# Kernel tuning notes

Hardware: AMD Instinct MI355X
Metric: run time of the kernel (lower is better)

The kernel has to match this reference:

```python
import jax, jax.numpy as jnp
import numpy as np

N_NODES = 100000
N_EDGES = 1000000  # even: first half = 'in' direction, second half = 'out' (inverse) direction
H = 128
N_REL = 200        # num_relations (for rel_labels embedding)
N_RELG = 100       # num_rel_graph; edge_type in [0, 2*N_RELG)
N_GRAPHS = 256
N_CLS = 2


def _glorot(key, shape):
    s = (6.0 / (shape[0] + shape[1])) ** 0.5
    return jax.random.uniform(key, shape, jnp.float32, -s, s)


def setup_inputs() -> dict:
    key = jax.random.key(0)
    ks = jax.random.split(key, 32)
    inp = {}
    inp['x'] = jax.random.normal(ks[0], (N_NODES, H), jnp.float32)
    inp['edge_index'] = jax.random.randint(ks[1], (2, N_EDGES), 0, N_NODES)
    inp['edge_type'] = jax.random.randint(ks[2], (N_EDGES,), 0, 2 * N_RELG)
    inp['batch'] = jnp.sort(jax.random.randint(ks[3], (N_NODES,), 0, N_GRAPHS))
    inp['rel_labels'] = jax.random.randint(ks[4], (N_GRAPHS,), 0, N_REL)
    inp['drop_prob'] = 0  # eval mode -> dropout is identity
    # learned parameters
    inp['rel_emb_table'] = jax.random.normal(ks[5], (N_REL, H), jnp.float32)
    inp['rel_graph_emb'] = _glorot(ks[6], (N_RELG, H))
    i = 7
    for l in (1, 2, 3):
        for nm in ('w_in', 'w_out', 'w_loop', 'w_rel'):
            inp[f'{nm}{l}'] = _glorot(ks[i], (H, H)); i += 1
        inp[f'loop_rel{l}'] = _glorot(ks[i], (1, H)); i += 1
        inp[f'b{l}'] = jnp.zeros((H,), jnp.float32)
    inp['lin_w'] = _glorot(ks[i], (2 * H, N_CLS))
    inp['lin_b'] = jnp.zeros((N_CLS,), jnp.float32)
    return inp


def _conv(x, edge_index, edge_type, rel, w_in, w_out, w_loop, w_rel, loop_rel, b):
    """CompGCNConv with 'sub' composition, tanh activation (BN/dropout identity in eval)."""
    n = x.shape[0]
    rel_all = jnp.concatenate([rel, loop_rel], axis=0)  # append loop relation
    half = edge_index.shape[1] // 2

    def direction(idx, etyp, w):
        src, dst = idx[0], idx[1]
        # norm as in CompGCN: deg over row(src), norm = deg_inv[row]*deg_inv[col]
        deg = jax.ops.segment_sum(jnp.ones(src.shape[0], x.dtype), src, num_segments=n)
        dinv = jnp.where(deg > 0, deg ** -0.5, 0.0)
        norm = dinv[src] * dinv[dst]                      # [E/2]
        msg = ((x[src] - rel_all[etyp]) @ w) * norm[:, None]  # gather-compose-transform
        return jax.ops.segment_sum(msg, dst, num_segments=n)  # scatter-add

    in_res = direction(edge_index[:, :half], edge_type[:half], w_in)
    out_res = direction(edge_index[:, half:], edge_type[half:], w_out)
    loop_res = (x - rel_all[-1]) @ w_loop
    out = (in_res + out_res + loop_res) * (1.0 / 3.0) + b
    return jnp.tanh(out), (rel_all @ w_rel)[:-1]


def reference(x, rel_emb_table, rel_graph_emb,
              w_in1, w_out1, w_loop1, w_rel1, loop_rel1, b1,
              w_in2, w_out2, w_loop2, w_rel2, loop_rel2, b2,
              w_in3, w_out3, w_loop3, w_rel3, loop_rel3, b3,
              lin_w, lin_b, edge_index, edge_type, batch, rel_labels, drop_prob):
    rel_embs = rel_emb_table[rel_labels]                   # [G, H]
    r = jnp.concatenate([rel_graph_emb, -rel_graph_emb], axis=0)  # [2*N_RELG, H]
    x, r = _conv(x, edge_index, edge_type, r, w_in1, w_out1, w_loop1, w_rel1, loop_rel1, b1)
    x = jax.nn.relu(x)
    x, r = _conv(x, edge_index, edge_type, r, w_in2, w_out2, w_loop2, w_rel2, loop_rel2, b2)
    x = jax.nn.relu(x)
    x, r = _conv(x, edge_index, edge_type, r, w_in3, w_out3, w_loop3, w_rel3, loop_rel3, b3)
    # global mean pool over graphs
    sums = jax.ops.segment_sum(x, batch, num_segments=N_GRAPHS)
    cnt = jax.ops.segment_sum(jnp.ones(batch.shape[0], x.dtype), batch, num_segments=N_GRAPHS)
    x = sums / jnp.maximum(cnt, 1.0)[:, None]              # [G, H]
    x = jnp.concatenate([x, rel_embs], axis=1)             # [G, 2H]
    # dropout identity (eval); final linear
    return x @ lin_w + lin_b                               # [G, 2]
```

## Files before the change

### kernel.cpp

```cpp
#include <hip/hip_runtime.h>
#include <hip/hip_bf16.h>
#include <math.h>

#define N_NODES 100000
#define N_EDGES 1000000
#define HALF_E  500000
#define H       128
#define NG      256
#define RELROWS 201
#define NH      (N_NODES * H)
#define SCAN_NB 98
#define XPITCH  136
#define MMB     64

typedef __attribute__((ext_vector_type(8))) short bf16x8;
typedef __attribute__((ext_vector_type(4))) float f32x4;

__device__ __forceinline__ float bflo(unsigned p) { return __uint_as_float(p << 16); }
__device__ __forceinline__ float bfhi(unsigned p) { return __uint_as_float(p & 0xffff0000u); }
__device__ __forceinline__ unsigned packbf2(float a, float b) {
    unsigned ua = __float_as_uint(a), ub = __float_as_uint(b);
    ua = (ua + 0x7fffu + ((ua >> 16) & 1u)) >> 16;
    ub = (ub + 0x7fffu + ((ub >> 16) & 1u)) >> 16;
    return ua | (ub << 16);
}
__device__ __forceinline__ unsigned short packbf1(float a) {
    unsigned ua = __float_as_uint(a);
    return (unsigned short)((ua + 0x7fffu + ((ua >> 16) & 1u)) >> 16);
}

__global__ void deg_hist_kernel(const int* __restrict__ ei, float* deg_in, float* deg_out,
                                int* __restrict__ cnt_dst) {
    int e = blockIdx.x * 256 + threadIdx.x;
    if (e >= N_EDGES) return;
    int src = ei[e];
    int dst = ei[N_EDGES + e];
    if (e < HALF_E) atomicAdd(deg_in + src, 1.0f);
    else            atomicAdd(deg_out + src, 1.0f);
    atomicAdd(cnt_dst + dst, 1);
}

__global__ void dinv_kernel(float* a, float* b) {
    int i = blockIdx.x * 256 + threadIdx.x;
    if (i >= N_NODES) return;
    float d = a[i]; a[i] = d > 0.f ? rsqrtf(d) : 0.f;
    d = b[i];       b[i] = d > 0.f ? rsqrtf(d) : 0.f;
}

__global__ __launch_bounds__(1024) void scan1_kernel(const int* __restrict__ cnt,
                                                     int* __restrict__ excl,
                                                     int* __restrict__ bsum) {
    __shared__ int ps[1024];
    int t = threadIdx.x;
    int i = blockIdx.x * 1024 + t;
    int v = (i < N_NODES) ? cnt[i] : 0;
    ps[t] = v;
    __syncthreads();
    for (int off = 1; off < 1024; off <<= 1) {
        int u = (t >= off) ? ps[t - off] : 0;
        __syncthreads();
        ps[t] += u;
        __syncthreads();
    }
    if (i < N_NODES) excl[i] = ps[t] - v;
    if (t == 1023) bsum[blockIdx.x] = ps[t];
}

__global__ __launch_bounds__(128) void scan2_kernel(const int* __restrict__ bsum,
                                                    int* __restrict__ boff,
                                                    int* __restrict__ rowptr) {
    __shared__ int ps[128];
    int t = threadIdx.x;
    int v = (t < SCAN_NB) ? bsum[t] : 0;
    ps[t] = v;
    __syncthreads();
    for (int off = 1; off < 128; off <<= 1) {
        int u = (t >= off) ? ps[t - off] : 0;
        __syncthreads();
        ps[t] += u;
        __syncthreads();
    }
    if (t < SCAN_NB) boff[t] = ps[t] - v;
    if (t == 127) rowptr[N_NODES] = ps[t];
}

__global__ __launch_bounds__(1024) void scan3_kernel(const int* __restrict__ excl,
                                                     const int* __restrict__ boff,
                                                     int* __restrict__ rowptr,
                                                     int* __restrict__ rfill) {
    int t = threadIdx.x;
    int i = blockIdx.x * 1024 + t;
    if (i >= N_NODES) return;
    int r = excl[i] + boff[blockIdx.x];
    rowptr[i] = r;
    rfill[i] = r;
}

__global__ void fill_kernel(const int* __restrict__ ei, const int* __restrict__ etype,
                            const float* __restrict__ dinv_in, const float* __restrict__ dinv_out,
                            int* __restrict__ rfill, int* __restrict__ meta,
                            float* __restrict__ csr_nrm) {
    int e = blockIdx.x * 256 + threadIdx.x;
    if (e >= N_EDGES) return;
    int s = ei[e], d = ei[N_EDGES + e];
    int t = etype[e];
    bool isin = (e < HALF_E);
    const float* dv = isin ? dinv_in : dinv_out;
    float nv = dv[s] * dv[d];
    int j = atomicAdd(rfill + d, 1);
    int src2 = s + (isin ? 0 : N_NODES);
    int typ2 = t + (isin ? 0 : 200);
    meta[j] = src2 | (typ2 << 18);
    csr_nrm[j] = nv;
}

__global__ void cnt_bs_kernel(const int* __restrict__ batch, float* __restrict__ cnt) {
    int g = blockIdx.x * 64 + threadIdx.x;
    if (g >= NG) return;
    int lo = 0, hi = N_NODES;
    while (lo < hi) { int mid = (lo + hi) >> 1; if (batch[mid] < g) lo = mid + 1; else hi = mid; }
    int start = lo;
    lo = 0; hi = N_NODES;
    while (lo < hi) { int mid = (lo + hi) >> 1; if (batch[mid] < g + 1) lo = mid + 1; else hi = mid; }
    cnt[g] = (float)(lo - start);
}

__global__ void rel_build_kernel(const float* __restrict__ rge, const float* __restrict__ rbuf,
                                 const float* __restrict__ loop_rel, float* __restrict__ relA, int layer) {
    int i = blockIdx.x;
    int j = threadIdx.x;
    float v;
    if (i == 200)          v = loop_rel[j];
    else if (layer == 1)   v = (i < 100) ? rge[i * H + j] : -rge[(i - 100) * H + j];
    else                   v = rbuf[i * H + j];
    relA[i * H + j] = v;
}

__global__ void rel_mm_kernel(const float* __restrict__ relA,
                              const float* __restrict__ wIn, const float* __restrict__ wOut,
                              const float* __restrict__ wRel, const float* __restrict__ wLoop,
                              unsigned short* __restrict__ RWh, float* __restrict__ rbuf,
                              float* __restrict__ lwl) {
    __shared__ float a[H];
    int i = blockIdx.x, j = threadIdx.x;
    a[j] = relA[i * H + j];
    __syncthreads();
    float s_in = 0.f, s_out = 0.f, s_rel = 0.f, s_loop = 0.f;
    for (int k = 0; k < H; k++) {
        float av = a[k];
        s_in  += av * wIn [k * H + j];
        s_out += av * wOut[k * H + j];
        s_rel += av * wRel[k * H + j];
        s_loop += av * wLoop[k * H + j];
    }
    if (i < 200) {
        RWh[i * H + j] = packbf1(s_in);
        RWh[(200 + i) * H + j] = packbf1(s_out);
        rbuf[i * H + j] = s_rel;
    }
    if (i == 200) lwl[j] = s_loop;
}

struct WPtrs { const float* p[9]; };
__global__ __launch_bounds__(256) void wpack_kernel(WPtrs wp, unsigned short* __restrict__ Bp) {
    int iw = blockIdx.y;
    const float* W = wp.p[iw];
    unsigned short* out = Bp + (size_t)iw * 16384;
    int t = blockIdx.x * 256 + threadIdx.x;
    int nt = t >> 8, kk = (t >> 6) & 3, lane = t & 63;
    int n = nt * 16 + (lane & 15);
    int k0 = kk * 32 + (lane >> 4) * 8;
    unsigned p[4];
    for (int j = 0; j < 4; j++)
        p[j] = packbf2(W[(k0 + 2 * j) * H + n], W[(k0 + 2 * j + 1) * H + n]);
    *(uint4*)(out + ((size_t)(nt * 4 + kk) * 64 + lane) * 8) = make_uint4(p[0], p[1], p[2], p[3]);
}

__global__ __launch_bounds__(256) void mm_mfma_kernel(const float* __restrict__ Xf,
                                                      const unsigned short* __restrict__ Xh,
                                                      int xf32,
                                                      const unsigned short* __restrict__ Bpack,
                                                      const float* __restrict__ lwl,
                                                      unsigned short* __restrict__ QRh,
                                                      unsigned short* __restrict__ Sb) {
    __shared__ unsigned short xt[MMB * XPITCH];
    int tid = threadIdx.x;
    int row0 = blockIdx.x * MMB;
    int nrows = min(MMB, N_NODES - row0);
    if (xf32) {
        for (int t = 0; t < 8; t++) {
            int idx = tid + t * 256;
            int r = idx >> 5, c4 = (idx & 31) * 4;
            if (r < nrows) {
                float4 v = *(const float4*)(Xf + (size_t)(row0 + r) * H + c4);
                *(uint2*)(xt + r * XPITCH + c4) = make_uint2(packbf2(v.x, v.y), packbf2(v.z, v.w));
            }
        }
    } else {
        for (int t = 0; t < 4; t++) {
            int idx = tid + t * 256;
            int r = idx >> 4, c8 = (idx & 15) * 8;
            if (r < nrows)
                *(uint4*)(xt + r * XPITCH + c8) = *(const uint4*)(Xh + (size_t)(row0 + r) * H + c8);
        }
    }
    __syncthreads();

    int wave = tid >> 6, lane = tid & 63;
    int m0w = wave * 16;
    int q = lane >> 4, ml = lane & 15;
    bf16x8 afrag[4];
    for (int kk = 0; kk < 4; kk++)
        afrag[kk] = *(const bf16x8*)(xt + (m0w + ml) * XPITCH + kk * 32 + q * 8);
    int grow_base = row0 + m0w + q * 4;
    for (int w = 0; w < 3; w++) {
        for (int nt = 0; nt < 8; nt++) {
            const unsigned short* bp = Bpack + (((size_t)(w * 8 + nt) * 4) * 64 + lane) * 8;
            f32x4 acc = {0.f, 0.f, 0.f, 0.f};
            for (int kk = 0; kk < 4; kk++) {
                bf16x8 bfrag = *(const bf16x8*)(bp + (size_t)kk * 512);
                acc = __builtin_amdgcn_mfma_f32_16x16x32_bf16(afrag[kk], bfrag, acc, 0, 0, 0);
            }
            int col = nt * 16 + ml;
            if (w < 2) {
                size_t rbase = (w == 0) ? 0 : (size_t)N_NODES;
                for (int reg = 0; reg < 4; reg++) {
                    int grow = grow_base + reg;
                    if (grow < N_NODES)
                        QRh[(rbase + grow) * H + col] = packbf1(acc[reg]);
                }
            } else {
                float sub = lwl[col];
                for (int reg = 0; reg < 4; reg++) {
                    int grow = grow_base + reg;
                    if (grow < N_NODES)
                        Sb[(size_t)grow * H + col] = packbf1(acc[reg] - sub);
                }
            }
        }
    }
}

__global__ __launch_bounds__(256) void gather_kernel(const int* __restrict__ rowptr,
                                                     const int* __restrict__ meta,
                                                     const float* __restrict__ csr_nrm,
                                                     const unsigned* __restrict__ QRh,
                                                     const unsigned* __restrict__ RWh,
                                                     const float* __restrict__ b,
                                                     unsigned* __restrict__ Sb,
                                                     const int* __restrict__ batch,
                                                     float* __restrict__ pool, int mode) {
    int v = blockIdx.x * 4 + (threadIdx.x >> 6);
    if (v >= N_NODES) return;
    int lane = threadIdx.x & 63;
    int c = lane * 2;
    int jb = rowptr[v], je = rowptr[v + 1];
    unsigned sv = Sb[(size_t)v * 64 + lane];
    float2 acc = make_float2(bflo(sv), bfhi(sv));
    int j = jb;
    for (; j + 3 < je; j += 4) {
        int m0 = meta[j], m1 = meta[j + 1], m2 = meta[j + 2], m3 = meta[j + 3];
        float n0 = csr_nrm[j], n1 = csr_nrm[j + 1], n2 = csr_nrm[j + 2], n3 = csr_nrm[j + 3];
        unsigned q0 = QRh[(size_t)(m0 & 0x3FFFF) * 64 + lane];
        unsigned r0 = RWh[(size_t)(m0 >> 18) * 64 + lane];
        unsigned q1 = QRh[(size_t)(m1 & 0x3FFFF) * 64 + lane];
        unsigned r1 = RWh[(size_t)(m1 >> 18) * 64 + lane];
        unsigned q2 = QRh[(size_t)(m2 & 0x3FFFF) * 64 + lane];
        unsigned r2 = RWh[(size_t)(m2 >> 18) * 64 + lane];
        unsigned q3 = QRh[(size_t)(m3 & 0x3FFFF) * 64 + lane];
        unsigned r3 = RWh[(size_t)(m3 >> 18) * 64 + lane];
        acc.x += (bflo(q0) - bflo(r0)) * n0; acc.y += (bfhi(q0) - bfhi(r0)) * n0;
        acc.x += (bflo(q1) - bflo(r1)) * n1; acc.y += (bfhi(q1) - bfhi(r1)) * n1;
        acc.x += (bflo(q2) - bflo(r2)) * n2; acc.y += (bfhi(q2) - bfhi(r2)) * n2;
        acc.x += (bflo(q3) - bflo(r3)) * n3; acc.y += (bfhi(q3) - bfhi(r3)) * n3;
    }
    for (; j < je; j++) {
        int m0 = meta[j];
        float n0 = csr_nrm[j];
        unsigned q0 = QRh[(size_t)(m0 & 0x3FFFF) * 64 + lane];
        unsigned r0 = RWh[(size_t)(m0 >> 18) * 64 + lane];
        acc.x += (bflo(q0) - bflo(r0)) * n0; acc.y += (bfhi(q0) - bfhi(r0)) * n0;
    }
    float v0 = tanhf(acc.x * (1.f / 3.f) + b[c]);
    float v1 = tanhf(acc.y * (1.f / 3.f) + b[c + 1]);
    if (mode == 0) {
        v0 = fmaxf(v0, 0.f); v1 = fmaxf(v1, 0.f);
        Sb[(size_t)v * 64 + lane] = packbf2(v0, v1);
    } else {
        int g = batch[v];
        atomicAdd(pool + g * H + c,     v0);
        atomicAdd(pool + g * H + c + 1, v1);
    }
}

__global__ void final_kernel(const float* __restrict__ pool, const float* __restrict__ cnt,
                             const float* __restrict__ rel_table, const int* __restrict__ rel_labels,
                             const float* __restrict__ lin_w, const float* __restrict__ lin_b,
                             float* __restrict__ out) {
    int g = blockIdx.x;
    int lane = threadIdx.x;
    float inv = 1.f / fmaxf(cnt[g], 1.f);
    const float* rrow = rel_table + (size_t)rel_labels[g] * H;
    float p0 = 0.f, p1 = 0.f;
    for (int c = lane; c < H; c += 64) {
        float m = pool[g * H + c] * inv;
        p0 += m * lin_w[c * 2 + 0];
        p1 += m * lin_w[c * 2 + 1];
        float rv = rrow[c];
        p0 += rv * lin_w[(H + c) * 2 + 0];
        p1 += rv * lin_w[(H + c) * 2 + 1];
    }
    for (int off = 32; off; off >>= 1) {
        p0 += __shfl_down(p0, off);
        p1 += __shfl_down(p1, off);
    }
    if (lane == 0) {
        out[g * 2 + 0] = p0 + lin_b[0];
        out[g * 2 + 1] = p1 + lin_b[1];
    }
}

extern "C" void kernel_launch(void* const* d_in, const int* in_sizes, int n_in,
                              void* d_out, int out_size, void* d_ws, size_t ws_size,
                              hipStream_t stream) {
    const float* x          = (const float*)d_in[0];
    const int*   ei         = (const int*)  d_in[1];
    const int*   etype      = (const int*)  d_in[2];
    const int*   batch      = (const int*)  d_in[3];
    const int*   rel_labels = (const int*)  d_in[4];
    const float* rel_table  = (const float*)d_in[6];
    const float* rge        = (const float*)d_in[7];
    const float* lin_w      = (const float*)d_in[26];
    const float* lin_b      = (const float*)d_in[27];
    float* out = (float*)d_out;

    float* ws       = (float*)d_ws;
    float* dinv_in  = ws;
    float* dinv_out = dinv_in + N_NODES;
    float* pool     = dinv_out + N_NODES;
    float* cnt      = pool + NG * H;
    float* relA     = cnt + NG;
    float* rbuf     = relA + RELROWS * H;
    float* lwl      = rbuf + 200 * H;
    float* csr_nrm  = lwl + 3 * H;
    int*   rowptr   = (int*)(csr_nrm + N_EDGES);
    int*   rfill    = rowptr + N_NODES + 1;
    int*   cnt_dst  = rfill + N_NODES;
    int*   meta     = cnt_dst + N_NODES;
    int*   excl     = meta + N_EDGES;
    int*   bsum     = excl + N_NODES;
    int*   boff     = bsum + SCAN_NB;
    unsigned* QRh   = (unsigned*)(boff + SCAN_NB + 2);
    unsigned* Sb    = QRh + (size_t)NH;
    unsigned* RWh   = Sb + (size_t)NH / 2;
    unsigned short* Bpack = (unsigned short*)(RWh + 3 * 400 * 64);

    hipMemsetAsync(dinv_in, 0, (size_t)(2 * N_NODES + NG * H + NG) * sizeof(float), stream);
    hipMemsetAsync(cnt_dst, 0, (size_t)N_NODES * sizeof(int), stream);

    deg_hist_kernel<<<(N_EDGES + 255) / 256, 256, 0, stream>>>(ei, dinv_in, dinv_out, cnt_dst);
    dinv_kernel    <<<(N_NODES + 255) / 256, 256, 0, stream>>>(dinv_in, dinv_out);
    scan1_kernel   <<<SCAN_NB, 1024, 0, stream>>>(cnt_dst, excl, bsum);
    scan2_kernel   <<<1, 128, 0, stream>>>(bsum, boff, rowptr);
    scan3_kernel   <<<SCAN_NB, 1024, 0, stream>>>(excl, boff, rowptr, rfill);
    fill_kernel    <<<(N_EDGES + 255) / 256, 256, 0, stream>>>(ei, etype, dinv_in, dinv_out,
                                                               rfill, meta, csr_nrm);
    cnt_bs_kernel  <<<NG / 64, 64, 0, stream>>>(batch, cnt);

    WPtrs wp;
    for (int l = 0; l < 3; l++) {
        wp.p[l * 3 + 0] = (const float*)d_in[8 + 6 * l + 0];
        wp.p[l * 3 + 1] = (const float*)d_in[8 + 6 * l + 1];
        wp.p[l * 3 + 2] = (const float*)d_in[8 + 6 * l + 2];
    }
    wpack_kernel<<<dim3(8, 9), 256, 0, stream>>>(wp, Bpack);

    for (int l = 0; l < 3; l++) {
        const float* wIn   = (const float*)d_in[8 + 6 * l + 0];
        const float* wOut  = (const float*)d_in[8 + 6 * l + 1];
        const float* wLoop = (const float*)d_in[8 + 6 * l + 2];
        const float* wRel  = (const float*)d_in[8 + 6 * l + 3];
        const float* lrel  = (const float*)d_in[8 + 6 * l + 4];
        rel_build_kernel<<<RELROWS, H, 0, stream>>>(rge, rbuf, lrel, relA, l + 1);
        rel_mm_kernel   <<<RELROWS, H, 0, stream>>>(relA, wIn, wOut, wRel, wLoop,
                                                    (unsigned short*)(RWh + (size_t)l * 400 * 64),
                                                    rbuf, lwl + l * H);
    }

    int mm_grid = (N_NODES + MMB - 1) / MMB;
    for (int l = 0; l < 3; l++) {
        const float* bl = (const float*)d_in[8 + 6 * l + 5];
        mm_mfma_kernel<<<mm_grid, 256, 0, stream>>>(x, (const unsigned short*)Sb, (l == 0) ? 1 : 0,
                                                    Bpack + (size_t)l * 3 * 16384, lwl + l * H,
                                                    (unsigned short*)QRh, (unsigned short*)Sb);
        gather_kernel<<<N_NODES / 4, 256, 0, stream>>>(rowptr, meta, csr_nrm,
                                                       QRh, RWh + (size_t)l * 400 * 64, bl,
                                                       Sb, batch, pool, (l == 2) ? 1 : 0);
    }

    final_kernel<<<NG, 64, 0, stream>>>(pool, cnt, rel_table, rel_labels, lin_w, lin_b, out);
}
```

Measured before the change: 771.2 us.

## Pack CSR meta/norm into int2 and gather 16-byte rows with 16 lanes per node

New measurement: 1.243 ms. +61.1%, slower.

```diff
diff --git a/kernel.cpp b/kernel.cpp
--- a/kernel.cpp
+++ b/kernel.cpp
@@ -98,8 +98,7 @@
 
 __global__ void fill_kernel(const int* __restrict__ ei, const int* __restrict__ etype,
                             const float* __restrict__ dinv_in, const float* __restrict__ dinv_out,
-                            int* __restrict__ rfill, int* __restrict__ meta,
-                            float* __restrict__ csr_nrm) {
+                            int* __restrict__ rfill, int2* __restrict__ csr_mn) {
     int e = blockIdx.x * 256 + threadIdx.x;
     if (e >= N_EDGES) return;
     int s = ei[e], d = ei[N_EDGES + e];
@@ -110,8 +109,7 @@
     int j = atomicAdd(rfill + d, 1);
     int src2 = s + (isin ? 0 : N_NODES);
     int typ2 = t + (isin ? 0 : 200);
-    meta[j] = src2 | (typ2 << 18);
-    csr_nrm[j] = nv;
+    csr_mn[j] = make_int2(src2 | (typ2 << 18), __float_as_int(nv));
 }
 
 __global__ void cnt_bs_kernel(const int* __restrict__ batch, float* __restrict__ cnt) {
@@ -241,55 +239,63 @@
     }
 }
 
+#define ACC8(qv, rv, n) \
+    acc[0] += (bflo(qv.x) - bflo(rv.x)) * n; acc[1] += (bfhi(qv.x) - bfhi(rv.x)) * n; \
+    acc[2] += (bflo(qv.y) - bflo(rv.y)) * n; acc[3] += (bfhi(qv.y) - bfhi(rv.y)) * n; \
+    acc[4] += (bflo(qv.z) - bflo(rv.z)) * n; acc[5] += (bfhi(qv.z) - bfhi(rv.z)) * n; \
+    acc[6] += (bflo(qv.w) - bflo(rv.w)) * n; acc[7] += (bfhi(qv.w) - bfhi(rv.w)) * n;
+
 __global__ __launch_bounds__(256) void gather_kernel(const int* __restrict__ rowptr,
-                                                     const int* __restrict__ meta,
-                                                     const float* __restrict__ csr_nrm,
+                                                     const int2* __restrict__ csr_mn,
                                                      const unsigned* __restrict__ QRh,
                                                      const unsigned* __restrict__ RWh,
                                                      const float* __restrict__ b,
                                                      unsigned* __restrict__ Sb,
                                                      const int* __restrict__ batch,
                                                      float* __restrict__ pool, int mode) {
-    int v = blockIdx.x * 4 + (threadIdx.x >> 6);
+    int tid = threadIdx.x;
+    int wave = tid >> 6, lane = tid & 63;
+    int sub = lane >> 4, sl = lane & 15;
+    int v = blockIdx.x * 16 + wave * 4 + sub;
     if (v >= N_NODES) return;
-    int lane = threadIdx.x & 63;
-    int c = lane * 2;
     int jb = rowptr[v], je = rowptr[v + 1];
-    unsigned sv = Sb[(size_t)v * 64 + lane];
-    float2 acc = make_float2(bflo(sv), bfhi(sv));
+    uint4 sv = *(const uint4*)(Sb + (size_t)v * 64 + sl * 4);
+    float acc[8];
+    acc[0] = bflo(sv.x); acc[1] = bfhi(sv.x);
+    acc[2] = bflo(sv.y); acc[3] = bfhi(sv.y);
+    acc[4] = bflo(sv.z); acc[5] = bfhi(sv.z);
+    acc[6] = bflo(sv.w); acc[7] = bfhi(sv.w);
     int j = jb;
-    for (; j + 3 < je; j += 4) {
-        int m0 = meta[j], m1 = meta[j + 1], m2 = meta[j + 2], m3 = meta[j + 3];
-        float n0 = csr_nrm[j], n1 = csr_nrm[j + 1], n2 = csr_nrm[j + 2], n3 = csr_nrm[j + 3];
-        unsigned q0 = QRh[(size_t)(m0 & 0x3FFFF) * 64 + lane];
-        unsigned r0 = RWh[(size_t)(m0 >> 18) * 64 + lane];
-        unsigned q1 = QRh[(size_t)(m1 & 0x3FFFF) * 64 + lane];
-        unsigned r1 = RWh[(size_t)(m1 >> 18) * 64 + lane];
-        unsigned q2 = QRh[(size_t)(m2 & 0x3FFFF) * 64 + lane];
-        unsigned r2 = RWh[(size_t)(m2 >> 18) * 64 + lane];
-        unsigned q3 = QRh[(size_t)(m3 & 0x3FFFF) * 64 + lane];
-        unsigned r3 = RWh[(size_t)(m3 >> 18) * 64 + lane];
-        acc.x += (bflo(q0) - bflo(r0)) * n0; acc.y += (bfhi(q0) - bfhi(r0)) * n0;
-        acc.x += (bflo(q1) - bflo(r1)) * n1; acc.y += (bfhi(q1) - bfhi(r1)) * n1;
-        acc.x += (bflo(q2) - bflo(r2)) * n2; acc.y += (bfhi(q2) - bfhi(r2)) * n2;
-        acc.x += (bflo(q3) - bflo(r3)) * n3; acc.y += (bfhi(q3) - bfhi(r3)) * n3;
-    }
-    for (; j < je; j++) {
-        int m0 = meta[j];
-        float n0 = csr_nrm[j];
-        unsigned q0 = QRh[(size_t)(m0 & 0x3FFFF) * 64 + lane];
-        unsigned r0 = RWh[(size_t)(m0 >> 18) * 64 + lane];
-        acc.x += (bflo(q0) - bflo(r0)) * n0; acc.y += (bfhi(q0) - bfhi(r0)) * n0;
-    }
-    float v0 = tanhf(acc.x * (1.f / 3.f) + b[c]);
-    float v1 = tanhf(acc.y * (1.f / 3.f) + b[c + 1]);
+    for (; j + 1 < je; j += 2) {
+        int2 mn0 = csr_mn[j], mn1 = csr_mn[j + 1];
+        uint4 q0 = *(const uint4*)(QRh + (size_t)(mn0.x & 0x3FFFF) * 64 + sl * 4);
+        uint4 r0 = *(const uint4*)(RWh + (size_t)((unsigned)mn0.x >> 18) * 64 + sl * 4);
+        uint4 q1 = *(const uint4*)(QRh + (size_t)(mn1.x & 0x3FFFF) * 64 + sl * 4);
+        uint4 r1 = *(const uint4*)(RWh + (size_t)((unsigned)mn1.x >> 18) * 64 + sl * 4);
+        float n0 = __int_as_float(mn0.y), n1 = __int_as_float(mn1.y);
+        ACC8(q0, r0, n0)
+        ACC8(q1, r1, n1)
+    }
+    if (j < je) {
+        int2 mn0 = csr_mn[j];
+        uint4 q0 = *(const uint4*)(QRh + (size_t)(mn0.x & 0x3FFFF) * 64 + sl * 4);
+        uint4 r0 = *(const uint4*)(RWh + (size_t)((unsigned)mn0.x >> 18) * 64 + sl * 4);
+        float n0 = __int_as_float(mn0.y);
+        ACC8(q0, r0, n0)
+    }
+    int c0 = sl * 8;
+    float vv[8];
+    for (int k = 0; k < 8; k++)
+        vv[k] = tanhf(acc[k] * (1.f / 3.f) + b[c0 + k]);
     if (mode == 0) {
-        v0 = fmaxf(v0, 0.f); v1 = fmaxf(v1, 0.f);
-        Sb[(size_t)v * 64 + lane] = packbf2(v0, v1);
+        for (int k = 0; k < 8; k++) vv[k] = fmaxf(vv[k], 0.f);
+        uint4 o = make_uint4(packbf2(vv[0], vv[1]), packbf2(vv[2], vv[3]),
+                             packbf2(vv[4], vv[5]), packbf2(vv[6], vv[7]));
+        *(uint4*)(Sb + (size_t)v * 64 + sl * 4) = o;
     } else {
         int g = batch[v];
-        atomicAdd(pool + g * H + c,     v0);
-        atomicAdd(pool + g * H + c + 1, v1);
+        for (int k = 0; k < 8; k++)
+            atomicAdd(pool + g * H + c0 + k, vv[k]);
     }
 }
 
@@ -342,15 +348,14 @@
     float* relA     = cnt + NG;
     float* rbuf     = relA + RELROWS * H;
     float* lwl      = rbuf + 200 * H;
-    float* csr_nrm  = lwl + 3 * H;
-    int*   rowptr   = (int*)(csr_nrm + N_EDGES);
-    int*   rfill    = rowptr + N_NODES + 1;
+    int*   rowptr   = (int*)(lwl + 3 * H);
+    int*   rfill    = rowptr + N_NODES + 4;
     int*   cnt_dst  = rfill + N_NODES;
-    int*   meta     = cnt_dst + N_NODES;
-    int*   excl     = meta + N_EDGES;
+    int*   excl     = cnt_dst + N_NODES;
     int*   bsum     = excl + N_NODES;
-    int*   boff     = bsum + SCAN_NB;
-    unsigned* QRh   = (unsigned*)(boff + SCAN_NB + 2);
+    int*   boff     = bsum + 100;
+    int2*  csr_mn   = (int2*)(boff + 100);
+    unsigned* QRh   = (unsigned*)(csr_mn + N_EDGES);
     unsigned* Sb    = QRh + (size_t)NH;
     unsigned* RWh   = Sb + (size_t)NH / 2;
     unsigned short* Bpack = (unsigned short*)(RWh + 3 * 400 * 64);
@@ -364,7 +369,7 @@
     scan2_kernel   <<<1, 128, 0, stream>>>(bsum, boff, rowptr);
     scan3_kernel   <<<SCAN_NB, 1024, 0, stream>>>(excl, boff, rowptr, rfill);
     fill_kernel    <<<(N_EDGES + 255) / 256, 256, 0, stream>>>(ei, etype, dinv_in, dinv_out,
-                                                               rfill, meta, csr_nrm);
+                                                               rfill, csr_mn);
     cnt_bs_kernel  <<<NG / 64, 64, 0, stream>>>(batch, cnt);
 
     WPtrs wp;
@@ -393,9 +398,9 @@
         mm_mfma_kernel<<<mm_grid, 256, 0, stream>>>(x, (const unsigned short*)Sb, (l == 0) ? 1 : 0,
                                                     Bpack + (size_t)l * 3 * 16384, lwl + l * H,
                                                     (unsigned short*)QRh, (unsigned short*)Sb);
-        gather_kernel<<<N_NODES / 4, 256, 0, stream>>>(rowptr, meta, csr_nrm,
-                                                       QRh, RWh + (size_t)l * 400 * 64, bl,
-                                                       Sb, batch, pool, (l == 2) ? 1 : 0);
+        gather_kernel<<<N_NODES / 16, 256, 0, stream>>>(rowptr, csr_mn,
+                                                        QRh, RWh + (size_t)l * 400 * 64, bl,
+                                                        Sb, batch, pool, (l == 2) ? 1 : 0);
     }
 
     final_kernel<<<NG, 64, 0, stream>>>(pool, cnt, rel_table, rel_labels, lin_w, lin_b, out);
```
